# Optimization experiments

Hardware: AMD Instinct MI355X
Metric: run time of the kernel (lower is better)

The kernel has to match this reference:

```python
import jax, jax.numpy as jnp
import numpy as np

E = 16          # number of experts/gates accumulated so far
B = 32768       # batch of tokens
LATENT = 128    # latent_dim
HID = 64        # hidden_dim
CLASSES = 10


def setup_inputs() -> dict:
    key = jax.random.key(0)
    ks = jax.random.split(key, 8)
    x = jax.random.normal(ks[0], (B, 1, 28, 28), dtype=jnp.float32)
    # hard routing: each token assigned to exactly one expert (argmin of recon errors)
    assign = jax.random.randint(ks[1], (B,), 0, E)
    mask = (jnp.arange(E)[:, None] == assign[None, :])  # [E, B] bool, one-hot per column
    latent = jax.random.normal(ks[2], (E, B, LATENT), dtype=jnp.float32)
    s1 = 1.0 / np.sqrt(LATENT)
    s2 = 1.0 / np.sqrt(HID)
    W1 = jax.random.normal(ks[3], (E, LATENT, HID), dtype=jnp.float32) * s1
    b1 = jnp.zeros((E, HID), dtype=jnp.float32)
    W2 = jax.random.normal(ks[4], (E, HID, HID), dtype=jnp.float32) * s2
    b2 = jnp.zeros((E, HID), dtype=jnp.float32)
    W3 = jax.random.normal(ks[5], (E, HID, CLASSES), dtype=jnp.float32) * s2
    b3 = jnp.zeros((E, CLASSES), dtype=jnp.float32)
    return {"x": x, "mask": mask, "latent": latent,
            "W1": W1, "b1": b1, "W2": W2, "b2": b2, "W3": W3, "b3": b3}


def reference(x, mask, latent, W1, b1, W2, b2, W3, b3):
    # Each expert e sees its OWN latent representation latent[e]; the torch code
    # gathers masked rows, runs ExpertMLP_e, and scatters into a zero logits tensor.
    # With an exclusive (one-hot per token) mask this equals a masked sum of
    # per-expert outputs; unrouted tokens stay zero, matching torch.zeros init.
    h = jax.nn.relu(jnp.einsum('ebl,elh->ebh', latent, W1) + b1[:, None, :])
    h = jax.nn.relu(jnp.einsum('ebh,ehk->ebk', h, W2) + b2[:, None, :])
    out = jnp.einsum('ebh,ehc->ebc', h, W3) + b3[:, None, :]  # [E, B, C]
    logits = jnp.sum(jnp.where(mask[:, :, None], out, jnp.zeros((), out.dtype)), axis=0)
    return logits  # [B, CLASSES]
```

## Files before the change

### kernel.cpp

```cpp
#include <hip/hip_runtime.h>
#include <hip/hip_bf16.h>
#include <cstdint>
#include <cstddef>

#define NE 16
#define NB 32768
#define LATENT 128
#define HID 64
#define CLASSES 10
#define BPE 32
#define TPB 256

__global__ void probe_kernel(const unsigned char* __restrict__ mask_bytes,
                             int* __restrict__ flag) {
    int tid = threadIdx.x;
    if (tid < 32) {
        int b = 1 + 4 * tid;
        int nz = 0;
        for (int e = 0; e < NE; ++e) nz |= mask_bytes[(size_t)e * NB + b];
        if (nz) atomicOr(flag, 1);
    }
}

__global__ void assign_kernel(const void* __restrict__ mask,
                              const int* __restrict__ flag,
                              int* __restrict__ counts,
                              unsigned short* __restrict__ lists) {
    int b = blockIdx.x * blockDim.x + threadIdx.x;
    if (b >= NB) return;
    int mode = *flag;
    int myE = 0;
    if (mode) {
        const unsigned char* m = (const unsigned char*)mask;
        for (int e = 0; e < NE; ++e)
            if (m[(size_t)e * NB + b]) { myE = e; break; }
    } else {
        const int* m = (const int*)mask;
        for (int e = 0; e < NE; ++e)
            if (m[(size_t)e * NB + b] != 0) { myE = e; break; }
    }
    int pos = atomicAdd(&counts[myE], 1);
    lists[myE * NB + pos] = (unsigned short)b;
}

__global__ __launch_bounds__(TPB, 2) void expert_kernel(
    const float* __restrict__ latent,
    const float* __restrict__ W1, const float* __restrict__ b1,
    const float* __restrict__ W2, const float* __restrict__ b2,
    const float* __restrict__ W3, const float* __restrict__ b3,
    const int* __restrict__ counts,
    const unsigned short* __restrict__ lists,
    float* __restrict__ out)
{
    __shared__ float sW1[LATENT * HID];
    __shared__ float sW2[HID * HID];
    __shared__ float sW3[HID * CLASSES + 8];
    __shared__ float sB1[HID], sB2[HID], sB3[16];
    __shared__ float sX[4][4][LATENT];

    const int e    = blockIdx.x / BPE;
    const int blk  = blockIdx.x % BPE;
    const int tid  = threadIdx.x;
    const int wave = tid >> 6;
    const int lane = tid & 63;

    {
        const float* g = W1 + (size_t)e * LATENT * HID;
        for (int i = tid * 4; i < LATENT * HID; i += TPB * 4)
            *(float4*)&sW1[i] = *(const float4*)&g[i];
        g = W2 + (size_t)e * HID * HID;
        for (int i = tid * 4; i < HID * HID; i += TPB * 4)
            *(float4*)&sW2[i] = *(const float4*)&g[i];
        g = W3 + (size_t)e * HID * CLASSES;
        for (int i = tid * 4; i < HID * CLASSES; i += TPB * 4)
            *(float4*)&sW3[i] = *(const float4*)&g[i];
        if (tid < HID) {
            sB1[tid] = b1[e * HID + tid];
            sB2[tid] = b2[e * HID + tid];
        }
        if (tid < 16) sB3[tid] = (tid < CLASSES) ? b3[e * CLASSES + tid] : 0.f;
    }
    __syncthreads();

    const int cnt = counts[e];
    if (cnt == 0) return;
    const int ntiles = (cnt + 15) >> 4;
    const unsigned short* mylist = lists + e * NB;

    for (int tile = blk; tile < ntiles; tile += BPE) {
        const int base = tile * 16;

        {
            int s = tid >> 4, p = tid & 15;
            int idx = base + s;
            int tok = mylist[idx < cnt ? idx : 0];
            const float4* src =
                (const float4*)(latent + ((size_t)e * NB + tok) * LATENT + p * 8);
            float4 v0 = src[0], v1 = src[1];
            float4* dst = (float4*)&sX[s >> 2][s & 3][p * 8];
            dst[0] = v0; dst[1] = v1;
        }
        __syncthreads();

        float a0 = sB1[lane], a1 = a0, a2 = a0, a3 = a0;
        for (int l = 0; l < LATENT; l += 4) {
            float w0 = sW1[(l + 0) * HID + lane];
            float w1 = sW1[(l + 1) * HID + lane];
            float w2 = sW1[(l + 2) * HID + lane];
            float w3 = sW1[(l + 3) * HID + lane];
            float4 x0 = *(const float4*)&sX[wave][0][l];
            float4 x1 = *(const float4*)&sX[wave][1][l];
            float4 x2 = *(const float4*)&sX[wave][2][l];
            float4 x3 = *(const float4*)&sX[wave][3][l];
            a0 += x0.x * w0 + x0.y * w1 + x0.z * w2 + x0.w * w3;
            a1 += x1.x * w0 + x1.y * w1 + x1.z * w2 + x1.w * w3;
            a2 += x2.x * w0 + x2.y * w1 + x2.z * w2 + x2.w * w3;
            a3 += x3.x * w0 + x3.y * w1 + x3.z * w2 + x3.w * w3;
        }
        a0 = fmaxf(a0, 0.f); a1 = fmaxf(a1, 0.f);
        a2 = fmaxf(a2, 0.f); a3 = fmaxf(a3, 0.f);
        sX[wave][0][lane] = a0; sX[wave][1][lane] = a1;
        sX[wave][2][lane] = a2; sX[wave][3][lane] = a3;
        __syncthreads();

        float c0 = sB2[lane], c1 = c0, c2 = c0, c3 = c0;
        for (int h = 0; h < HID; h += 4) {
            float w0 = sW2[(h + 0) * HID + lane];
            float w1 = sW2[(h + 1) * HID + lane];
            float w2 = sW2[(h + 2) * HID + lane];
            float w3 = sW2[(h + 3) * HID + lane];
            float4 x0 = *(const float4*)&sX[wave][0][h];
            float4 x1 = *(const float4*)&sX[wave][1][h];
            float4 x2 = *(const float4*)&sX[wave][2][h];
            float4 x3 = *(const float4*)&sX[wave][3][h];
            c0 += x0.x * w0 + x0.y * w1 + x0.z * w2 + x0.w * w3;
            c1 += x1.x * w0 + x1.y * w1 + x1.z * w2 + x1.w * w3;
            c2 += x2.x * w0 + x2.y * w1 + x2.z * w2 + x2.w * w3;
            c3 += x3.x * w0 + x3.y * w1 + x3.z * w2 + x3.w * w3;
        }
        c0 = fmaxf(c0, 0.f); c1 = fmaxf(c1, 0.f);
        c2 = fmaxf(c2, 0.f); c3 = fmaxf(c3, 0.f);
        sX[wave][0][lane] = c0; sX[wave][1][lane] = c1;
        sX[wave][2][lane] = c2; sX[wave][3][lane] = c3;
        __syncthreads();

        {
            int t = lane >> 4, c = lane & 15;
            float acc = sB3[c];
            for (int h = 0; h < HID; ++h)
                acc += sX[wave][t][h] * sW3[h * CLASSES + c];
            int slot = base + wave * 4 + t;
            if (c < CLASSES && slot < cnt) {
                int tok = mylist[slot];
                out[(size_t)tok * CLASSES + c] = acc;
            }
        }
        __syncthreads();
    }
}

extern "C" void kernel_launch(void* const* d_in, const int* in_sizes, int n_in,
                              void* d_out, int out_size, void* d_ws, size_t ws_size,
                              hipStream_t stream) {
    const void*  mask   = d_in[1];
    const float* latent = (const float*)d_in[2];
    const float* W1 = (const float*)d_in[3];
    const float* b1 = (const float*)d_in[4];
    const float* W2 = (const float*)d_in[5];
    const float* b2 = (const float*)d_in[6];
    const float* W3 = (const float*)d_in[7];
    const float* b3 = (const float*)d_in[8];
    float* out = (float*)d_out;

    int* flag   = (int*)d_ws;
    int* counts = (int*)((char*)d_ws + 64);
    unsigned short* lists = (unsigned short*)((char*)d_ws + 128);

    hipMemsetAsync(d_ws, 0, 128, stream);
    probe_kernel<<<1, 64, 0, stream>>>((const unsigned char*)mask, flag);
    assign_kernel<<<NB / 256, 256, 0, stream>>>(mask, flag, counts, lists);
    expert_kernel<<<NE * BPE, TPB, 0, stream>>>(latent, W1, b1, W2, b2, W3, b3,
                                                counts, lists, out);
}
```

Before: 484.4 us.

## Restructure expert MLP to per-token-per-lane register tiles with scalar weight loads

Measured after the change: 515.7 us. 6.5% more time.

```diff
diff --git a/kernel.cpp b/kernel.cpp
--- a/kernel.cpp
+++ b/kernel.cpp
@@ -8,27 +8,27 @@
 #define LATENT 128
 #define HID 64
 #define CLASSES 10
-#define BPE 32
-#define TPB 256
+#define WPE 32
 
-__global__ void probe_kernel(const unsigned char* __restrict__ mask_bytes,
-                             int* __restrict__ flag) {
-    int tid = threadIdx.x;
+__global__ void assign_kernel(const void* __restrict__ mask,
+                              int* __restrict__ counts,
+                              unsigned short* __restrict__ lists) {
+    __shared__ int sMode;
+    const int tid = threadIdx.x;
+    if (tid == 0) sMode = 0;
+    __syncthreads();
     if (tid < 32) {
+        const unsigned char* mb = (const unsigned char*)mask;
         int b = 1 + 4 * tid;
         int nz = 0;
-        for (int e = 0; e < NE; ++e) nz |= mask_bytes[(size_t)e * NB + b];
-        if (nz) atomicOr(flag, 1);
+        for (int e = 0; e < NE; ++e) nz |= mb[(size_t)e * NB + b];
+        if (nz) atomicOr(&sMode, 1);
     }
-}
+    __syncthreads();
+    const int mode = sMode;
 
-__global__ void assign_kernel(const void* __restrict__ mask,
-                              const int* __restrict__ flag,
-                              int* __restrict__ counts,
-                              unsigned short* __restrict__ lists) {
-    int b = blockIdx.x * blockDim.x + threadIdx.x;
+    int b = blockIdx.x * blockDim.x + tid;
     if (b >= NB) return;
-    int mode = *flag;
     int myE = 0;
     if (mode) {
         const unsigned char* m = (const unsigned char*)mask;
@@ -43,7 +43,7 @@
     lists[myE * NB + pos] = (unsigned short)b;
 }
 
-__global__ __launch_bounds__(TPB, 2) void expert_kernel(
+__global__ __launch_bounds__(128) void expert_kernel(
     const float* __restrict__ latent,
     const float* __restrict__ W1, const float* __restrict__ b1,
     const float* __restrict__ W2, const float* __restrict__ b2,
@@ -52,107 +52,93 @@
     const unsigned short* __restrict__ lists,
     float* __restrict__ out)
 {
-    __shared__ float sW1[LATENT * HID];
-    __shared__ float sW2[HID * HID];
-    __shared__ float sW3[HID * CLASSES + 8];
-    __shared__ float sB1[HID], sB2[HID], sB3[16];
-    __shared__ float sX[4][4][LATENT];
+    __shared__ float sX[LATENT * 64];
 
-    const int e    = blockIdx.x / BPE;
-    const int blk  = blockIdx.x % BPE;
-    const int tid  = threadIdx.x;
-    const int wave = tid >> 6;
+    const int e   = blockIdx.x / WPE;
+    const int blk = blockIdx.x % WPE;
+    const int tid = threadIdx.x;
     const int lane = tid & 63;
-
-    {
-        const float* g = W1 + (size_t)e * LATENT * HID;
-        for (int i = tid * 4; i < LATENT * HID; i += TPB * 4)
-            *(float4*)&sW1[i] = *(const float4*)&g[i];
-        g = W2 + (size_t)e * HID * HID;
-        for (int i = tid * 4; i < HID * HID; i += TPB * 4)
-            *(float4*)&sW2[i] = *(const float4*)&g[i];
-        g = W3 + (size_t)e * HID * CLASSES;
-        for (int i = tid * 4; i < HID * CLASSES; i += TPB * 4)
-            *(float4*)&sW3[i] = *(const float4*)&g[i];
-        if (tid < HID) {
-            sB1[tid] = b1[e * HID + tid];
-            sB2[tid] = b2[e * HID + tid];
-        }
-        if (tid < 16) sB3[tid] = (tid < CLASSES) ? b3[e * CLASSES + tid] : 0.f;
-    }
-    __syncthreads();
+    const int jh  = __builtin_amdgcn_readfirstlane(tid >> 6);
 
     const int cnt = counts[e];
-    if (cnt == 0) return;
-    const int ntiles = (cnt + 15) >> 4;
+    const int ntiles = (cnt + 63) >> 6;
     const unsigned short* mylist = lists + e * NB;
 
-    for (int tile = blk; tile < ntiles; tile += BPE) {
-        const int base = tile * 16;
+    const float* w1e = W1 + (size_t)e * LATENT * HID + jh * 32;
+    const float* w2e = W2 + (size_t)e * HID * HID + jh * 32;
+    const float* w3e = W3 + (size_t)e * HID * CLASSES + jh * 5;
+    const float* b1e = b1 + e * HID + jh * 32;
+    const float* b2e = b2 + e * HID + jh * 32;
+    const float* b3e = b3 + e * CLASSES + jh * 5;
+
+    for (int tile = blk; tile < ntiles; tile += WPE) {
+        const int base = tile * 64;
 
         {
-            int s = tid >> 4, p = tid & 15;
+            const int s = tid & 63, half = tid >> 6;
             int idx = base + s;
-            int tok = mylist[idx < cnt ? idx : 0];
-            const float4* src =
-                (const float4*)(latent + ((size_t)e * NB + tok) * LATENT + p * 8);
-            float4 v0 = src[0], v1 = src[1];
-            float4* dst = (float4*)&sX[s >> 2][s & 3][p * 8];
-            dst[0] = v0; dst[1] = v1;
+            if (idx >= cnt) idx = cnt - 1;
+            const int tok = mylist[idx];
+            const float4* src = (const float4*)
+                (latent + ((size_t)e * NB + tok) * LATENT + half * 64);
+            #pragma unroll
+            for (int i = 0; i < 16; ++i) {
+                float4 v = src[i];
+                int l = half * 64 + i * 4;
+                sX[(l + 0) * 64 + s] = v.x;
+                sX[(l + 1) * 64 + s] = v.y;
+                sX[(l + 2) * 64 + s] = v.z;
+                sX[(l + 3) * 64 + s] = v.w;
+            }
         }
         __syncthreads();
 
-        float a0 = sB1[lane], a1 = a0, a2 = a0, a3 = a0;
-        for (int l = 0; l < LATENT; l += 4) {
-            float w0 = sW1[(l + 0) * HID + lane];
-            float w1 = sW1[(l + 1) * HID + lane];
-            float w2 = sW1[(l + 2) * HID + lane];
-            float w3 = sW1[(l + 3) * HID + lane];
-            float4 x0 = *(const float4*)&sX[wave][0][l];
-            float4 x1 = *(const float4*)&sX[wave][1][l];
-            float4 x2 = *(const float4*)&sX[wave][2][l];
-            float4 x3 = *(const float4*)&sX[wave][3][l];
-            a0 += x0.x * w0 + x0.y * w1 + x0.z * w2 + x0.w * w3;
-            a1 += x1.x * w0 + x1.y * w1 + x1.z * w2 + x1.w * w3;
-            a2 += x2.x * w0 + x2.y * w1 + x2.z * w2 + x2.w * w3;
-            a3 += x3.x * w0 + x3.y * w1 + x3.z * w2 + x3.w * w3;
+        float acc[32];
+        #pragma unroll
+        for (int j = 0; j < 32; ++j) acc[j] = b1e[j];
+        for (int l = 0; l < LATENT; ++l) {
+            float x = sX[l * 64 + lane];
+            const float* wr = w1e + l * HID;
+            #pragma unroll
+            for (int j = 0; j < 32; ++j) acc[j] = fmaf(x, wr[j], acc[j]);
         }
-        a0 = fmaxf(a0, 0.f); a1 = fmaxf(a1, 0.f);
-        a2 = fmaxf(a2, 0.f); a3 = fmaxf(a3, 0.f);
-        sX[wave][0][lane] = a0; sX[wave][1][lane] = a1;
-        sX[wave][2][lane] = a2; sX[wave][3][lane] = a3;
+        __syncthreads();
+        #pragma unroll
+        for (int j = 0; j < 32; ++j)
+            sX[(jh * 32 + j) * 64 + lane] = fmaxf(acc[j], 0.f);
         __syncthreads();
 
-        float c0 = sB2[lane], c1 = c0, c2 = c0, c3 = c0;
-        for (int h = 0; h < HID; h += 4) {
-            float w0 = sW2[(h + 0) * HID + lane];
-            float w1 = sW2[(h + 1) * HID + lane];
-            float w2 = sW2[(h + 2) * HID + lane];
-            float w3 = sW2[(h + 3) * HID + lane];
-            float4 x0 = *(const float4*)&sX[wave][0][h];
-            float4 x1 = *(const float4*)&sX[wave][1][h];
-            float4 x2 = *(const float4*)&sX[wave][2][h];
-            float4 x3 = *(const float4*)&sX[wave][3][h];
-            c0 += x0.x * w0 + x0.y * w1 + x0.z * w2 + x0.w * w3;
-            c1 += x1.x * w0 + x1.y * w1 + x1.z * w2 + x1.w * w3;
-            c2 += x2.x * w0 + x2.y * w1 + x2.z * w2 + x2.w * w3;
-            c3 += x3.x * w0 + x3.y * w1 + x3.z * w2 + x3.w * w3;
+        float acc2[32];
+        #pragma unroll
+        for (int j = 0; j < 32; ++j) acc2[j] = b2e[j];
+        for (int l = 0; l < HID; ++l) {
+            float x = sX[l * 64 + lane];
+            const float* wr = w2e + l * HID;
+            #pragma unroll
+            for (int j = 0; j < 32; ++j) acc2[j] = fmaf(x, wr[j], acc2[j]);
         }
-        c0 = fmaxf(c0, 0.f); c1 = fmaxf(c1, 0.f);
-        c2 = fmaxf(c2, 0.f); c3 = fmaxf(c3, 0.f);
-        sX[wave][0][lane] = c0; sX[wave][1][lane] = c1;
-        sX[wave][2][lane] = c2; sX[wave][3][lane] = c3;
+        __syncthreads();
+        #pragma unroll
+        for (int j = 0; j < 32; ++j)
+            sX[(jh * 32 + j) * 64 + lane] = fmaxf(acc2[j], 0.f);
         __syncthreads();
 
+        float a3[5];
+        #pragma unroll
+        for (int c = 0; c < 5; ++c) a3[c] = b3e[c];
+        for (int l = 0; l < HID; ++l) {
+            float x = sX[l * 64 + lane];
+            const float* wr = w3e + l * CLASSES;
+            #pragma unroll
+            for (int c = 0; c < 5; ++c) a3[c] = fmaf(x, wr[c], a3[c]);
+        }
         {
-            int t = lane >> 4, c = lane & 15;
-            float acc = sB3[c];
-            for (int h = 0; h < HID; ++h)
-                acc += sX[wave][t][h] * sW3[h * CLASSES + c];
-            int slot = base + wave * 4 + t;
-            if (c < CLASSES && slot < cnt) {
+            int slot = base + lane;
+            if (slot < cnt) {
                 int tok = mylist[slot];
-                out[(size_t)tok * CLASSES + c] = acc;
+                float* o = out + (size_t)tok * CLASSES + jh * 5;
+                #pragma unroll
+                for (int c = 0; c < 5; ++c) o[c] = a3[c];
             }
         }
         __syncthreads();
@@ -172,13 +158,11 @@
     const float* b3 = (const float*)d_in[8];
     float* out = (float*)d_out;
 
-    int* flag   = (int*)d_ws;
-    int* counts = (int*)((char*)d_ws + 64);
+    int* counts = (int*)d_ws;
     unsigned short* lists = (unsigned short*)((char*)d_ws + 128);
 
     hipMemsetAsync(d_ws, 0, 128, stream);
-    probe_kernel<<<1, 64, 0, stream>>>((const unsigned char*)mask, flag);
-    assign_kernel<<<NB / 256, 256, 0, stream>>>(mask, flag, counts, lists);
-    expert_kernel<<<NE * BPE, TPB, 0, stream>>>(latent, W1, b1, W2, b2, W3, b3,
+    assign_kernel<<<NB / 256, 256, 0, stream>>>(mask, counts, lists);
+    expert_kernel<<<NE * WPE, 128, 0, stream>>>(latent, W1, b1, W2, b2, W3, b3,
                                                 counts, lists, out);
 }
```
